# Optimization experiments

Hardware: AMD Instinct MI355X
Metric: run time of the kernel (lower is better)

Reference implementation:

```python
import jax, jax.numpy as jnp
import numpy as np

B, N, D = 4, 2048, 256
H, DA, DL = 4, 64, 64          # heads, q/k dim per head, u/v dim per head
NUM_BUCKETS = 128
LN_EPS = 1e-5


def _layernorm(x, g, b):
    mu = jnp.mean(x, axis=-1, keepdims=True)
    var = jnp.var(x, axis=-1, keepdims=True)
    return (x - mu) * jax.lax.rsqrt(var + LN_EPS) * g + b


def setup_inputs() -> dict:
    key = jax.random.key(0)
    ks = jax.random.split(key, 8)
    x = jax.random.normal(ks[0], (B, N, D), jnp.float32)
    lengths = jax.random.randint(ks[1], (B,), 1, N + 1).astype(jnp.int64)
    timestamps = jnp.sort(
        jax.random.randint(ks[2], (B, N), 0, 10_000_000), axis=1
    ).astype(jnp.int64)
    F_uvqk = H * (2 * DL + 2 * DA)
    W_uvqk = jax.random.normal(ks[3], (D, F_uvqk), jnp.float32) * 0.02
    b_uvqk = jnp.zeros((F_uvqk,), jnp.float32)
    W_o = jax.random.normal(ks[4], (H * DL, D), jnp.float32) * 0.02
    b_o = jnp.zeros((D,), jnp.float32)
    ln_in_g = jnp.ones((D,), jnp.float32)
    ln_in_b = jnp.zeros((D,), jnp.float32)
    ln_attn_g = jnp.ones((H * DL,), jnp.float32)
    ln_attn_b = jnp.zeros((H * DL,), jnp.float32)
    w_pos = jax.random.normal(ks[5], (2 * N - 1,), jnp.float32) * 0.02
    w_ts = jax.random.normal(ks[6], (NUM_BUCKETS + 1,), jnp.float32) * 0.02
    return dict(x=x, W_uvqk=W_uvqk, b_uvqk=b_uvqk, W_o=W_o, b_o=b_o,
                ln_in_g=ln_in_g, ln_in_b=ln_in_b,
                ln_attn_g=ln_attn_g, ln_attn_b=ln_attn_b,
                w_pos=w_pos, w_ts=w_ts,
                lengths=lengths, timestamps=timestamps)


def reference(x, W_uvqk, b_uvqk, W_o, b_o, ln_in_g, ln_in_b,
              ln_attn_g, ln_attn_b, w_pos, w_ts, lengths, timestamps):
    # HSTU jagged transduction unit (padded + mask representation).
    nx = _layernorm(x, ln_in_g, ln_in_b)                       # [B,N,D]
    uvqk = jax.nn.silu(nx @ W_uvqk + b_uvqk)                   # fused projection
    u, v, q, k = jnp.split(
        uvqk, [H * DL, 2 * H * DL, 2 * H * DL + H * DA], axis=-1)
    q = q.reshape(B, N, H, DA)
    k = k.reshape(B, N, H, DA)
    v = v.reshape(B, N, H, DL)
    qk = jnp.einsum('bnhd,bmhd->bhnm', q, k)                   # [B,H,N,N]

    # relative position + bucketed relative timestamp bias -> [B,N,N]
    pos = jnp.arange(N)
    pos_bias = w_pos[pos[:, None] - pos[None, :] + (N - 1)]    # [N,N]
    diff = timestamps[:, :, None] - timestamps[:, None, :]     # [B,N,N] int
    bucket = jnp.clip(
        (jnp.log(jnp.maximum(jnp.abs(diff).astype(jnp.float32), 1.0)) / 0.301)
        .astype(jnp.int32), 0, NUM_BUCKETS)
    bias = pos_bias[None] + w_ts[bucket]                       # [B,N,N]

    # non-softmax HSTU attention: silu(scores)/N, causal + valid-key mask
    attn = jax.nn.silu(qk + bias[:, None, :, :]) * (1.0 / N)
    causal = pos[:, None] >= pos[None, :]                      # [N,N]
    valid = pos[None, :] < lengths[:, None]                    # [B,N]
    mask = causal[None, None, :, :] & valid[:, None, None, :]
    attn = jnp.where(mask, attn, 0.0)

    av = jnp.einsum('bhnm,bmhd->bnhd', attn, v).reshape(B, N, H * DL)
    out = (_layernorm(av, ln_attn_g, ln_attn_b) * u) @ W_o + b_o + x
    out = jnp.where(valid[:, :, None], out, 0.0)               # zero padded rows
    return out
```

## Files before the change

### kernel.cpp

```cpp
#include <hip/hip_runtime.h>
#include <stdint.h>

#define BB 4
#define NN 2048
#define DD 256
#define HH 4

typedef __attribute__((ext_vector_type(8))) __bf16 bf16x8;
typedef __attribute__((ext_vector_type(4))) float f32x4;
typedef __attribute__((ext_vector_type(8))) unsigned short u16x8;
typedef __attribute__((ext_vector_type(4))) unsigned short u16x4;

__device__ __forceinline__ unsigned short f2bf(float f) {
  union { float f; uint32_t u; } v; v.f = f;
  uint32_t r = v.u + 0x7fffu + ((v.u >> 16) & 1u);
  return (unsigned short)(r >> 16);
}
__device__ __forceinline__ bf16x8 ld8(const unsigned short* p) {
  return __builtin_bit_cast(bf16x8, *(const u16x8*)p);
}
__device__ __forceinline__ f32x4 mfma16(bf16x8 a, bf16x8 b, f32x4 c) {
  return __builtin_amdgcn_mfma_f32_16x16x32_bf16(a, b, c, 0, 0, 0);
}
__device__ __forceinline__ float silu_f(float x) {
  return x / (1.0f + __expf(-x));
}

__global__ __launch_bounds__(256) void k_prep_w(const float* __restrict__ Wu,
                                                const float* __restrict__ Wo,
                                                unsigned short* __restrict__ Wu_t,
                                                unsigned short* __restrict__ Wo_t) {
  int idx = blockIdx.x * 256 + threadIdx.x;
  if (idx < 1024 * 256) {
    int f = idx >> 8, d = idx & 255;
    Wu_t[idx] = f2bf(Wu[d * 1024 + f]);
  } else {
    int i = idx - 1024 * 256;
    int f = i >> 8, d = i & 255;
    Wo_t[i] = f2bf(Wo[d * 256 + f]);
  }
}

__global__ __launch_bounds__(256) void k_ln_in(const float* __restrict__ x,
                                               const float* __restrict__ g,
                                               const float* __restrict__ be,
                                               unsigned short* __restrict__ nx) {
  int wave = threadIdx.x >> 6, lane = threadIdx.x & 63;
  int row = blockIdx.x * 4 + wave;
  const float4 v = *(const float4*)(x + (size_t)row * DD + lane * 4);
  float s = v.x + v.y + v.z + v.w;
  float sq = v.x * v.x + v.y * v.y + v.z * v.z + v.w * v.w;
  #pragma unroll
  for (int o = 32; o; o >>= 1) { s += __shfl_xor(s, o); sq += __shfl_xor(sq, o); }
  float mean = s * (1.0f / DD);
  float var = sq * (1.0f / DD) - mean * mean;
  float rstd = rsqrtf(var + 1e-5f);
  const float4 gv = *(const float4*)(g + lane * 4);
  const float4 bv = *(const float4*)(be + lane * 4);
  u16x4 o4;
  o4[0] = f2bf((v.x - mean) * rstd * gv.x + bv.x);
  o4[1] = f2bf((v.y - mean) * rstd * gv.y + bv.y);
  o4[2] = f2bf((v.z - mean) * rstd * gv.z + bv.z);
  o4[3] = f2bf((v.w - mean) * rstd * gv.w + bv.w);
  *(u16x4*)(nx + (size_t)row * DD + lane * 4) = o4;
}

__global__ __launch_bounds__(256) void k_gemm_uvqk(const unsigned short* __restrict__ nx,
                                                   const unsigned short* __restrict__ Wu_t,
                                                   const float* __restrict__ b_uvqk,
                                                   float* __restrict__ u,
                                                   unsigned short* __restrict__ v_tmp,
                                                   unsigned short* __restrict__ q_t,
                                                   unsigned short* __restrict__ k_t) {
  __shared__ unsigned short As[128 * 72];
  __shared__ unsigned short Bs[128 * 72];
  int tid = threadIdx.x, lane = tid & 63, w = tid >> 6;
  int wr = w >> 1, wc = w & 1, c = lane & 15, g = lane >> 4;
  int rblk = blockIdx.x >> 3, cblk = blockIdx.x & 7;
  int R0 = rblk * 128, C0 = cblk * 128;
  f32x4 acc[4][4] = {};
  for (int ks = 0; ks < 4; ++ks) {
    __syncthreads();
    #pragma unroll
    for (int it = 0; it < 4; ++it) {
      int task = tid + it * 256, row = task >> 3, ch = task & 7;
      *(u16x8*)(As + row * 72 + ch * 8) =
          *(const u16x8*)(nx + (size_t)(R0 + row) * 256 + ks * 64 + ch * 8);
      *(u16x8*)(Bs + row * 72 + ch * 8) =
          *(const u16x8*)(Wu_t + (size_t)(C0 + row) * 256 + ks * 64 + ch * 8);
    }
    __syncthreads();
    #pragma unroll
    for (int kk = 0; kk < 2; ++kk) {
      int koff = kk * 32 + g * 8;
      bf16x8 af[4], bfr[4];
      #pragma unroll
      for (int rt = 0; rt < 4; ++rt) af[rt] = ld8(As + (wr * 64 + rt * 16 + c) * 72 + koff);
      #pragma unroll
      for (int ct = 0; ct < 4; ++ct) bfr[ct] = ld8(Bs + (wc * 64 + ct * 16 + c) * 72 + koff);
      #pragma unroll
      for (int rt = 0; rt < 4; ++rt)
        #pragma unroll
        for (int ct = 0; ct < 4; ++ct)
          acc[rt][ct] = mfma16(af[rt], bfr[ct], acc[rt][ct]);
    }
  }
  #pragma unroll
  for (int rt = 0; rt < 4; ++rt) {
    #pragma unroll
    for (int ct = 0; ct < 4; ++ct) {
      int F = C0 + wc * 64 + ct * 16 + c;
      float bb = b_uvqk[F];
      #pragma unroll
      for (int rr = 0; rr < 4; ++rr) {
        int R = R0 + wr * 64 + rt * 16 + g * 4 + rr;
        float pre = acc[rt][ct][rr] + bb;
        float sv = silu_f(pre);
        int b = R >> 11, n = R & 2047;
        if (F < 256) {
          u[(size_t)R * 256 + F] = sv;
        } else if (F < 512) {
          v_tmp[(size_t)R * 256 + (F - 256)] = f2bf(sv);
        } else if (F < 768) {
          int h = (F - 512) >> 6, d = (F - 512) & 63;
          q_t[((size_t)((b << 2) + h) * 2048 + n) * 64 + d] = f2bf(sv);
        } else {
          int h = (F - 768) >> 6, d = (F - 768) & 63;
          k_t[((size_t)((b << 2) + h) * 2048 + n) * 64 + d] = f2bf(sv);
        }
      }
    }
  }
}

__global__ __launch_bounds__(256) void k_vtrans(const unsigned short* __restrict__ v_tmp,
                                                unsigned short* __restrict__ v_t) {
  __shared__ unsigned short T[64 * 72];
  int bi = blockIdx.x;
  int nch = bi & 31, h = (bi >> 5) & 3, b = bi >> 7;
  int n0 = nch * 64;
  int tid = threadIdx.x;
  #pragma unroll
  for (int it = 0; it < 2; ++it) {
    int task = tid + it * 256;
    int i = task >> 3, ch = task & 7;
    *(u16x8*)(T + i * 72 + ch * 8) =
        *(const u16x8*)(v_tmp + ((size_t)(b * 2048 + n0 + i)) * 256 + h * 64 + ch * 8);
  }
  __syncthreads();
  #pragma unroll
  for (int it = 0; it < 2; ++it) {
    int task = tid + it * 256;
    int d = task >> 3, ch = task & 7;
    u16x8 ov;
    #pragma unroll
    for (int uu = 0; uu < 8; ++uu) ov[uu] = T[(ch * 8 + uu) * 72 + d];
    *(u16x8*)(v_t + ((size_t)((b * 4 + h) * 64 + d)) * 2048 + n0 + ch * 8) = ov;
  }
}

__global__ __launch_bounds__(256) void k_attn(const unsigned short* __restrict__ q_t,
                                              const unsigned short* __restrict__ k_t,
                                              const unsigned short* __restrict__ v_t,
                                              const int* __restrict__ ts_raw,
                                              const int* __restrict__ lens_raw,
                                              const float* __restrict__ w_pos,
                                              const float* __restrict__ w_ts,
                                              float* __restrict__ av_out) {
  __shared__ float bias_s[16 * 68];
  __shared__ float P_s[4][16 * 68];
  int tid = threadIdx.x, lane = tid & 63, h = tid >> 6;
  int c = lane & 15, g = lane >> 4;
  int bi = blockIdx.x;
  int b = bi & 3, qt = 127 - (bi >> 2);
  int n0 = qt * 16;
  int stride = (lens_raw[1] == 0 && lens_raw[3] == 0) ? 2 : 1;
  int Lb = lens_raw[b * stride];
  const int* tsb = ts_raw + (size_t)b * 2048 * stride;
  const unsigned short* qp = q_t + (size_t)(b * 4 + h) * 2048 * 64;
  const unsigned short* kp = k_t + (size_t)(b * 4 + h) * 2048 * 64;
  const unsigned short* vp = v_t + (size_t)(b * 4 + h) * 64 * 2048;

  bf16x8 qf[2];
  qf[0] = ld8(qp + (size_t)(n0 + c) * 64 + g * 8);
  qf[1] = ld8(qp + (size_t)(n0 + c) * 64 + 32 + g * 8);
  f32x4 av[4] = {};
  int m_end = min(n0 + 16, Lb);
  for (int m0 = 0; m0 < m_end; m0 += 64) {
    #pragma unroll
    for (int it = 0; it < 4; ++it) {
      int e = tid + it * 256;
      int nl = e >> 6, ml = e & 63;
      int n = n0 + nl, m = m0 + ml;
      int dtv = tsb[n * stride] - tsb[m * stride];
      float ad = fmaxf(fabsf((float)dtv), 1.0f);
      int bk = (int)(logf(ad) / 0.301f);
      bk = bk > 128 ? 128 : bk;
      bias_s[nl * 68 + ml] = w_pos[n - m + 2047] + w_ts[bk];
    }
    __syncthreads();
    f32x4 s[4] = {};
    #pragma unroll
    for (int mt = 0; mt < 4; ++mt) {
      bf16x8 kf0 = ld8(kp + (size_t)(m0 + mt * 16 + c) * 64 + g * 8);
      bf16x8 kf1 = ld8(kp + (size_t)(m0 + mt * 16 + c) * 64 + 32 + g * 8);
      s[mt] = mfma16(qf[0], kf0, s[mt]);
      s[mt] = mfma16(qf[1], kf1, s[mt]);
    }
    float* Pw = P_s[h];
    #pragma unroll
    for (int mt = 0; mt < 4; ++mt) {
      #pragma unroll
      for (int rr = 0; rr < 4; ++rr) {
        int nl = g * 4 + rr, ml = mt * 16 + c;
        float sv = s[mt][rr] + bias_s[nl * 68 + ml];
        int n = n0 + nl, m = m0 + ml;
        float p = 0.0f;
        if (m <= n && m < Lb) p = silu_f(sv) * (1.0f / 2048.0f);
        Pw[nl * 68 + ml] = p;
      }
    }
    #pragma unroll
    for (int kk = 0; kk < 2; ++kk) {
      f32x4 plo = *(const f32x4*)(Pw + c * 68 + kk * 32 + g * 8);
      f32x4 phi = *(const f32x4*)(Pw + c * 68 + kk * 32 + g * 8 + 4);
      union { bf16x8 v; unsigned short e[8]; } pu;
      pu.e[0] = f2bf(plo.x); pu.e[1] = f2bf(plo.y);
      pu.e[2] = f2bf(plo.z); pu.e[3] = f2bf(plo.w);
      pu.e[4] = f2bf(phi.x); pu.e[5] = f2bf(phi.y);
      pu.e[6] = f2bf(phi.z); pu.e[7] = f2bf(phi.w);
      #pragma unroll
      for (int dt = 0; dt < 4; ++dt) {
        bf16x8 vf = ld8(vp + (size_t)(dt * 16 + c) * 2048 + m0 + kk * 32 + g * 8);
        av[dt] = mfma16(pu.v, vf, av[dt]);
      }
    }
    __syncthreads();
  }
  #pragma unroll
  for (int dt = 0; dt < 4; ++dt)
    #pragma unroll
    for (int rr = 0; rr < 4; ++rr) {
      int n = n0 + g * 4 + rr;
      av_out[((size_t)b * 2048 + n) * 256 + h * 64 + dt * 16 + c] = av[dt][rr];
    }
}

__global__ __launch_bounds__(256) void k_ln_attn(const float* __restrict__ av,
                                                 const float* __restrict__ u,
                                                 const float* __restrict__ g,
                                                 const float* __restrict__ be,
                                                 unsigned short* __restrict__ a2) {
  int wave = threadIdx.x >> 6, lane = threadIdx.x & 63;
  int row = blockIdx.x * 4 + wave;
  const float4 v = *(const float4*)(av + (size_t)row * DD + lane * 4);
  float s = v.x + v.y + v.z + v.w;
  float sq = v.x * v.x + v.y * v.y + v.z * v.z + v.w * v.w;
  #pragma unroll
  for (int o = 32; o; o >>= 1) { s += __shfl_xor(s, o); sq += __shfl_xor(sq, o); }
  float mean = s * (1.0f / DD);
  float var = sq * (1.0f / DD) - mean * mean;
  float rstd = rsqrtf(var + 1e-5f);
  const float4 gv = *(const float4*)(g + lane * 4);
  const float4 bv = *(const float4*)(be + lane * 4);
  const float4 uv = *(const float4*)(u + (size_t)row * DD + lane * 4);
  u16x4 o4;
  o4[0] = f2bf(((v.x - mean) * rstd * gv.x + bv.x) * uv.x);
  o4[1] = f2bf(((v.y - mean) * rstd * gv.y + bv.y) * uv.y);
  o4[2] = f2bf(((v.z - mean) * rstd * gv.z + bv.z) * uv.z);
  o4[3] = f2bf(((v.w - mean) * rstd * gv.w + bv.w) * uv.w);
  *(u16x4*)(a2 + (size_t)row * DD + lane * 4) = o4;
}

__global__ __launch_bounds__(256) void k_gemm_out(const unsigned short* __restrict__ a2,
                                                  const unsigned short* __restrict__ Wo_t,
                                                  const float* __restrict__ b_o,
                                                  const float* __restrict__ x,
                                                  const int* __restrict__ lens_raw,
                                                  float* __restrict__ out) {
  __shared__ unsigned short As[64 * 72];
  __shared__ unsigned short Bs[64 * 72];
  int tid = threadIdx.x, lane = tid & 63, w = tid >> 6;
  int wr = w >> 1, wc = w & 1, c = lane & 15, g = lane >> 4;
  int rblk = blockIdx.x >> 2, cblk = blockIdx.x & 3;
  int R0 = rblk * 64, C0 = cblk * 64;
  int stride = (lens_raw[1] == 0 && lens_raw[3] == 0) ? 2 : 1;
  f32x4 acc[2][2] = {};
  for (int ks = 0; ks < 4; ++ks) {
    __syncthreads();
    #pragma unroll
    for (int it = 0; it < 2; ++it) {
      int task = tid + it * 256, row = task >> 3, ch = task & 7;
      *(u16x8*)(As + row * 72 + ch * 8) =
          *(const u16x8*)(a2 + (size_t)(R0 + row) * 256 + ks * 64 + ch * 8);
      *(u16x8*)(Bs + row * 72 + ch * 8) =
          *(const u16x8*)(Wo_t + (size_t)(C0 + row) * 256 + ks * 64 + ch * 8);
    }
    __syncthreads();
    #pragma unroll
    for (int kk = 0; kk < 2; ++kk) {
      int koff = kk * 32 + g * 8;
      bf16x8 af[2], bfr[2];
      #pragma unroll
      for (int rt = 0; rt < 2; ++rt) af[rt] = ld8(As + (wr * 32 + rt * 16 + c) * 72 + koff);
      #pragma unroll
      for (int ct = 0; ct < 2; ++ct) bfr[ct] = ld8(Bs + (wc * 32 + ct * 16 + c) * 72 + koff);
      #pragma unroll
      for (int rt = 0; rt < 2; ++rt)
        #pragma unroll
        for (int ct = 0; ct < 2; ++ct)
          acc[rt][ct] = mfma16(af[rt], bfr[ct], acc[rt][ct]);
    }
  }
  #pragma unroll
  for (int rt = 0; rt < 2; ++rt) {
    #pragma unroll
    for (int ct = 0; ct < 2; ++ct) {
      int F = C0 + wc * 32 + ct * 16 + c;
      float bo = b_o[F];
      #pragma unroll
      for (int rr = 0; rr < 4; ++rr) {
        int R = R0 + wr * 32 + rt * 16 + g * 4 + rr;
        int b = R >> 11, n = R & 2047;
        int Lb = lens_raw[b * stride];
        float val = acc[rt][ct][rr] + bo + x[(size_t)R * 256 + F];
        out[(size_t)R * 256 + F] = (n < Lb) ? val : 0.0f;
      }
    }
  }
}

extern "C" void kernel_launch(void* const* d_in, const int* in_sizes, int n_in,
                              void* d_out, int out_size, void* d_ws, size_t ws_size,
                              hipStream_t stream) {
  const float* x        = (const float*)d_in[0];
  const float* W_uvqk   = (const float*)d_in[1];
  const float* b_uvqk   = (const float*)d_in[2];
  const float* W_o      = (const float*)d_in[3];
  const float* b_o      = (const float*)d_in[4];
  const float* ln_in_g  = (const float*)d_in[5];
  const float* ln_in_b  = (const float*)d_in[6];
  const float* ln_attn_g= (const float*)d_in[7];
  const float* ln_attn_b= (const float*)d_in[8];
  const float* w_pos    = (const float*)d_in[9];
  const float* w_ts     = (const float*)d_in[10];
  const int*   lengths  = (const int*)d_in[11];
  const int*   tstamps  = (const int*)d_in[12];
  float* out = (float*)d_out;

  char* ws = (char*)d_ws;
  size_t off = 0;
  auto alloc = [&](size_t bytes) -> void* {
    void* p = ws + off;
    off += (bytes + 255) & ~(size_t)255;
    return p;
  };
  unsigned short* Wu_t  = (unsigned short*)alloc(1024 * 256 * 2);
  unsigned short* Wo_t  = (unsigned short*)alloc(256 * 256 * 2);
  unsigned short* nx    = (unsigned short*)alloc((size_t)8192 * 256 * 2);
  float*          u     = (float*)alloc((size_t)8192 * 256 * 4);
  unsigned short* v_tmp = (unsigned short*)alloc((size_t)8192 * 256 * 2);
  unsigned short* v_t   = (unsigned short*)alloc((size_t)8192 * 256 * 2);
  unsigned short* q_t   = (unsigned short*)alloc((size_t)8192 * 256 * 2);
  unsigned short* k_t   = (unsigned short*)alloc((size_t)8192 * 256 * 2);
  float*          av    = (float*)alloc((size_t)8192 * 256 * 4);
  unsigned short* a2    = (unsigned short*)alloc((size_t)8192 * 256 * 2);

  k_prep_w<<<1280, 256, 0, stream>>>(W_uvqk, W_o, Wu_t, Wo_t);
  k_ln_in<<<2048, 256, 0, stream>>>(x, ln_in_g, ln_in_b, nx);
  k_gemm_uvqk<<<512, 256, 0, stream>>>(nx, Wu_t, b_uvqk, u, v_tmp, q_t, k_t);
  k_vtrans<<<512, 256, 0, stream>>>(v_tmp, v_t);
  k_attn<<<512, 256, 0, stream>>>(q_t, k_t, v_t, tstamps, lengths, w_pos, w_ts, av);
  k_ln_attn<<<2048, 256, 0, stream>>>(av, u, ln_attn_g, ln_attn_b, a2);
  k_gemm_out<<<512, 256, 0, stream>>>(a2, Wo_t, b_o, x, lengths, out);
}
```

Before: 253.2 us.

## Split attention KV range across blocks and compute bias in registers

The attention kernel splits the key range for query rows at or above 1024 into two chunks handled by separate blocks. This adds 256 blocks to even out the causal load imbalance, and the second partial sum is written to a buffer aliased onto the now-dead nx workspace. The LN-attn kernel adds the two partials. The timestamp/position bias is now computed per element in registers using a log2-based bucket formula, which removes the shared bias tile and both block barriers per KV step. P is stored in shared memory directly as bf16. Weight prep is rewritten as a shared-memory tiled transpose with vectorized loads and stores. Risks are the extra partial-sum traffic and possible bucket rounding differences at boundaries from the log2 rescale.

```diff
diff --git a/kernel.cpp b/kernel.cpp
--- a/kernel.cpp
+++ b/kernel.cpp
@@ -30,14 +30,28 @@
                                                 const float* __restrict__ Wo,
                                                 unsigned short* __restrict__ Wu_t,
                                                 unsigned short* __restrict__ Wo_t) {
-  int idx = blockIdx.x * 256 + threadIdx.x;
-  if (idx < 1024 * 256) {
-    int f = idx >> 8, d = idx & 255;
-    Wu_t[idx] = f2bf(Wu[d * 1024 + f]);
-  } else {
-    int i = idx - 1024 * 256;
-    int f = i >> 8, d = i & 255;
-    Wo_t[i] = f2bf(Wo[d * 256 + f]);
+  __shared__ float T[64][65];
+  int bi = blockIdx.x;
+  const float* src; unsigned short* dst; int F, f0, d0;
+  if (bi < 64) { src = Wu; dst = Wu_t; F = 1024; f0 = (bi >> 2) * 64; d0 = (bi & 3) * 64; }
+  else { int j = bi - 64; src = Wo; dst = Wo_t; F = 256; f0 = (j >> 2) * 64; d0 = (j & 3) * 64; }
+  int t = threadIdx.x;
+  int li = t >> 4;
+  int lj = (t & 15) * 4;
+  #pragma unroll
+  for (int it = 0; it < 4; ++it) {
+    int d = li + it * 16;
+    float4 v = *(const float4*)(src + (size_t)(d0 + d) * F + f0 + lj);
+    T[lj + 0][d] = v.x; T[lj + 1][d] = v.y; T[lj + 2][d] = v.z; T[lj + 3][d] = v.w;
+  }
+  __syncthreads();
+  #pragma unroll
+  for (int it = 0; it < 4; ++it) {
+    int f = li + it * 16;
+    u16x4 o;
+    o[0] = f2bf(T[f][lj + 0]); o[1] = f2bf(T[f][lj + 1]);
+    o[2] = f2bf(T[f][lj + 2]); o[3] = f2bf(T[f][lj + 3]);
+    *(u16x4*)(dst + (size_t)(f0 + f) * 256 + d0 + lj) = o;
   }
 }
 
@@ -166,13 +180,15 @@
                                               const int* __restrict__ lens_raw,
                                               const float* __restrict__ w_pos,
                                               const float* __restrict__ w_ts,
-                                              float* __restrict__ av_out) {
-  __shared__ float bias_s[16 * 68];
-  __shared__ float P_s[4][16 * 68];
+                                              float* __restrict__ avP0,
+                                              float* __restrict__ avP1) {
+  __shared__ unsigned short P_s[4][16 * 72];
   int tid = threadIdx.x, lane = tid & 63, h = tid >> 6;
   int c = lane & 15, g = lane >> 4;
   int bi = blockIdx.x;
-  int b = bi & 3, qt = 127 - (bi >> 2);
+  int b, qt, chunk;
+  if (bi < 512) { chunk = 0; b = bi & 3; qt = 127 - (bi >> 2); }
+  else { chunk = 1; int j = bi - 512; b = j & 3; qt = 127 - (j >> 2); }
   int n0 = qt * 16;
   int stride = (lens_raw[1] == 0 && lens_raw[3] == 0) ? 2 : 1;
   int Lb = lens_raw[b * stride];
@@ -181,79 +197,86 @@
   const unsigned short* kp = k_t + (size_t)(b * 4 + h) * 2048 * 64;
   const unsigned short* vp = v_t + (size_t)(b * 4 + h) * 64 * 2048;
 
-  bf16x8 qf[2];
-  qf[0] = ld8(qp + (size_t)(n0 + c) * 64 + g * 8);
-  qf[1] = ld8(qp + (size_t)(n0 + c) * 64 + 32 + g * 8);
+  int m_end = min(n0 + 16, Lb);
+  int kv_lo = chunk ? 1024 : 0;
+  int kv_hi = chunk ? m_end : min(m_end, 1024);
+
+  bf16x8 qf0 = ld8(qp + (size_t)(n0 + c) * 64 + g * 8);
+  bf16x8 qf1 = ld8(qp + (size_t)(n0 + c) * 64 + 32 + g * 8);
+  int tn[4];
+  #pragma unroll
+  for (int rr = 0; rr < 4; ++rr) tn[rr] = tsb[(n0 + g * 4 + rr) * stride];
+  unsigned short* Pw = &P_s[h][0];
   f32x4 av[4] = {};
-  int m_end = min(n0 + 16, Lb);
-  for (int m0 = 0; m0 < m_end; m0 += 64) {
-    #pragma unroll
-    for (int it = 0; it < 4; ++it) {
-      int e = tid + it * 256;
-      int nl = e >> 6, ml = e & 63;
-      int n = n0 + nl, m = m0 + ml;
-      int dtv = tsb[n * stride] - tsb[m * stride];
-      float ad = fmaxf(fabsf((float)dtv), 1.0f);
-      int bk = (int)(logf(ad) / 0.301f);
-      bk = bk > 128 ? 128 : bk;
-      bias_s[nl * 68 + ml] = w_pos[n - m + 2047] + w_ts[bk];
-    }
-    __syncthreads();
+
+  for (int m0 = kv_lo; m0 < kv_hi; m0 += 64) {
     f32x4 s[4] = {};
     #pragma unroll
     for (int mt = 0; mt < 4; ++mt) {
-      bf16x8 kf0 = ld8(kp + (size_t)(m0 + mt * 16 + c) * 64 + g * 8);
-      bf16x8 kf1 = ld8(kp + (size_t)(m0 + mt * 16 + c) * 64 + 32 + g * 8);
-      s[mt] = mfma16(qf[0], kf0, s[mt]);
-      s[mt] = mfma16(qf[1], kf1, s[mt]);
-    }
-    float* Pw = P_s[h];
+      const unsigned short* kr = kp + (size_t)(m0 + mt * 16 + c) * 64 + g * 8;
+      s[mt] = mfma16(qf0, ld8(kr), s[mt]);
+      s[mt] = mfma16(qf1, ld8(kr + 32), s[mt]);
+    }
     #pragma unroll
     for (int mt = 0; mt < 4; ++mt) {
+      int m = m0 + mt * 16 + c;
+      int tm = tsb[m * stride];
       #pragma unroll
       for (int rr = 0; rr < 4; ++rr) {
-        int nl = g * 4 + rr, ml = mt * 16 + c;
-        float sv = s[mt][rr] + bias_s[nl * 68 + ml];
-        int n = n0 + nl, m = m0 + ml;
-        float p = 0.0f;
-        if (m <= n && m < Lb) p = silu_f(sv) * (1.0f / 2048.0f);
-        Pw[nl * 68 + ml] = p;
+        int n = n0 + g * 4 + rr;
+        int dtv = tn[rr] - tm;
+        float ad = fmaxf(fabsf((float)dtv), 1.0f);
+        int bk = (int)(__log2f(ad) * 2.3028145f);
+        bk = bk > 128 ? 128 : bk;
+        float sv = s[mt][rr] + w_pos[n - m + 2047] + w_ts[bk];
+        float p = (m <= n && m < Lb) ? silu_f(sv) * (1.0f / 2048.0f) : 0.0f;
+        Pw[(g * 4 + rr) * 72 + mt * 16 + c] = f2bf(p);
       }
     }
     #pragma unroll
     for (int kk = 0; kk < 2; ++kk) {
-      f32x4 plo = *(const f32x4*)(Pw + c * 68 + kk * 32 + g * 8);
-      f32x4 phi = *(const f32x4*)(Pw + c * 68 + kk * 32 + g * 8 + 4);
-      union { bf16x8 v; unsigned short e[8]; } pu;
-      pu.e[0] = f2bf(plo.x); pu.e[1] = f2bf(plo.y);
-      pu.e[2] = f2bf(plo.z); pu.e[3] = f2bf(plo.w);
-      pu.e[4] = f2bf(phi.x); pu.e[5] = f2bf(phi.y);
-      pu.e[6] = f2bf(phi.z); pu.e[7] = f2bf(phi.w);
+      bf16x8 pa = ld8(Pw + c * 72 + kk * 32 + g * 8);
       #pragma unroll
       for (int dt = 0; dt < 4; ++dt) {
         bf16x8 vf = ld8(vp + (size_t)(dt * 16 + c) * 2048 + m0 + kk * 32 + g * 8);
-        av[dt] = mfma16(pu.v, vf, av[dt]);
-      }
-    }
-    __syncthreads();
-  }
-  #pragma unroll
-  for (int dt = 0; dt < 4; ++dt)
-    #pragma unroll
-    for (int rr = 0; rr < 4; ++rr) {
-      int n = n0 + g * 4 + rr;
-      av_out[((size_t)b * 2048 + n) * 256 + h * 64 + dt * 16 + c] = av[dt][rr];
-    }
-}
-
-__global__ __launch_bounds__(256) void k_ln_attn(const float* __restrict__ av,
+        av[dt] = mfma16(pa, vf, av[dt]);
+      }
+    }
+  }
+
+  if (chunk == 0) {
+    #pragma unroll
+    for (int dt = 0; dt < 4; ++dt)
+      #pragma unroll
+      for (int rr = 0; rr < 4; ++rr) {
+        int n = n0 + g * 4 + rr;
+        avP0[((size_t)(b * 2048 + n)) * 256 + h * 64 + dt * 16 + c] = av[dt][rr];
+      }
+  } else {
+    #pragma unroll
+    for (int dt = 0; dt < 4; ++dt)
+      #pragma unroll
+      for (int rr = 0; rr < 4; ++rr) {
+        int n = n0 + g * 4 + rr;
+        avP1[((size_t)(b * 1024 + (n - 1024))) * 256 + h * 64 + dt * 16 + c] = av[dt][rr];
+      }
+  }
+}
+
+__global__ __launch_bounds__(256) void k_ln_attn(const float* __restrict__ avP0,
+                                                 const float* __restrict__ avP1,
                                                  const float* __restrict__ u,
                                                  const float* __restrict__ g,
                                                  const float* __restrict__ be,
                                                  unsigned short* __restrict__ a2) {
   int wave = threadIdx.x >> 6, lane = threadIdx.x & 63;
   int row = blockIdx.x * 4 + wave;
-  const float4 v = *(const float4*)(av + (size_t)row * DD + lane * 4);
+  int n = row & 2047, b = row >> 11;
+  float4 v = *(const float4*)(avP0 + (size_t)row * DD + lane * 4);
+  if (n >= 1024) {
+    const float4 w = *(const float4*)(avP1 + ((size_t)(b * 1024 + (n - 1024))) * DD + lane * 4);
+    v.x += w.x; v.y += w.y; v.z += w.z; v.w += w.w;
+  }
   float s = v.x + v.y + v.z + v.w;
   float sq = v.x * v.x + v.y * v.y + v.z * v.z + v.w * v.w;
   #pragma unroll
@@ -363,14 +386,15 @@
   unsigned short* v_t   = (unsigned short*)alloc((size_t)8192 * 256 * 2);
   unsigned short* q_t   = (unsigned short*)alloc((size_t)8192 * 256 * 2);
   unsigned short* k_t   = (unsigned short*)alloc((size_t)8192 * 256 * 2);
-  float*          av    = (float*)alloc((size_t)8192 * 256 * 4);
+  float*          avP0  = (float*)alloc((size_t)8192 * 256 * 4);
   unsigned short* a2    = (unsigned short*)alloc((size_t)8192 * 256 * 2);
-
-  k_prep_w<<<1280, 256, 0, stream>>>(W_uvqk, W_o, Wu_t, Wo_t);
+  float*          avP1  = (float*)nx;
+
+  k_prep_w<<<80, 256, 0, stream>>>(W_uvqk, W_o, Wu_t, Wo_t);
   k_ln_in<<<2048, 256, 0, stream>>>(x, ln_in_g, ln_in_b, nx);
   k_gemm_uvqk<<<512, 256, 0, stream>>>(nx, Wu_t, b_uvqk, u, v_tmp, q_t, k_t);
   k_vtrans<<<512, 256, 0, stream>>>(v_tmp, v_t);
-  k_attn<<<512, 256, 0, stream>>>(q_t, k_t, v_t, tstamps, lengths, w_pos, w_ts, av);
-  k_ln_attn<<<2048, 256, 0, stream>>>(av, u, ln_attn_g, ln_attn_b, a2);
+  k_attn<<<768, 256, 0, stream>>>(q_t, k_t, v_t, tstamps, lengths, w_pos, w_ts, avP0, avP1);
+  k_ln_attn<<<2048, 256, 0, stream>>>(avP0, avP1, u, ln_attn_g, ln_attn_b, a2);
   k_gemm_out<<<512, 256, 0, stream>>>(a2, Wo_t, b_o, x, lengths, out);
 }
```

New measurement: 237.1 us. -6.4%, faster.
